# Performance work log

Hardware: AMD Instinct MI355X
Metric: run time of the kernel (lower is better)

Reference implementation:

```python
import jax, jax.numpy as jnp
import numpy as np

# LIF hyperparameters (from the torch module's `parameters` dict)
C = 1.0            # C_Osc
THR = 1.0          # v_Osc_threshold
BS = 256           # trials_per_stimulus
N = 512            # neurons_n
N_IN = 512         # n_in
TAU_SYN = 0.01     # tau_Osc_Ie
TAU_SYN_REC = 0.01 # tau_Osc_Irec
TAU_NEU = 0.02     # tau_Osc
GAIN_SYN = 1.0     # TDE_to_Osc_current
GAIN_SYN_REC = 0.5 # gain_syn_rec
DT = 0.001         # clock_sim
VR = 0.0           # reset_osc
I_MIN = 0.0        # I_minimum_osc
I_STEP = 0.01      # I_step_osc
REFRAC = 0.002     # refrac_Osc
REFR = REFRAC / DT # refractory period in steps
T = 500            # simulated timesteps


def spike(x):
    # SurrGradSpike.forward: hard threshold (surrogate grad only matters in bwd)
    return (x > 0.0).astype(x.dtype)


def setup_inputs() -> dict:
    key = jax.random.key(0)
    k1, k2, k3 = jax.random.split(key, 3)
    x = jax.random.uniform(k1, (T, BS, N_IN), dtype=jnp.float32)
    # train=True init: h1 ~ N(1, (std*0.5/sqrt(n_in))^2), r1 ~ N(0, same)
    std = 1.0 * 0.5 / np.sqrt(N_IN)
    h1 = 1.0 + std * jax.random.normal(k2, (N_IN, N), dtype=jnp.float32)
    r1 = std * jax.random.normal(k3, (N, N), dtype=jnp.float32)
    return {"x": x, "h1": h1, "r1": r1}


def reference(x, h1, r1):
    steady = I_MIN + I_STEP * jnp.arange(N, dtype=jnp.float32)  # [N]

    def step(state, x_t):
        V, Isyn, Irec, cnt, spk = state
        Isyn = Isyn - DT * Isyn / TAU_SYN + GAIN_SYN * (x_t @ h1)
        Irec = Irec - DT * Irec / TAU_SYN_REC + GAIN_SYN_REC * (spk @ r1)
        V = V + DT * (-V / TAU_NEU + (Isyn + Irec + steady) / C)
        V = jnp.maximum(V, 0.0)
        spk_new = spike(V - THR)
        cnt = REFR * spk_new + (1.0 - spk_new) * (cnt - 1.0)
        V = (1.0 - spk_new) * V * (cnt <= 0.0).astype(V.dtype) + spk_new * VR
        return (V, Isyn, Irec, cnt, spk_new), spk_new

    init = (
        jnp.ones((BS, N), jnp.float32),   # V
        jnp.zeros((BS, N), jnp.float32),  # Isyn
        jnp.zeros((BS, N), jnp.float32),  # Irec
        jnp.zeros((BS, N), jnp.float32),  # count_refr
        jnp.zeros((BS, N), jnp.float32),  # spk
    )
    _, spikes = jax.lax.scan(step, init, x)
    return spikes  # [T, BS, N]
```

## Files before the change

### kernel.cpp

```cpp
#include <hip/hip_runtime.h>

typedef __attribute__((ext_vector_type(8))) short short8;
typedef __attribute__((ext_vector_type(4))) float f32x4;

constexpr int BSZ = 256;
constexpr int NRN = 512;
constexpr int KIN = 512;
constexpr int TT  = 500;
constexpr int KT  = 32;
constexpr int BM2 = 64;
constexpr int NB2 = TT * BSZ / BM2;
constexpr int BM  = 128;
constexpr int BN  = 128;
constexpr int NBLK = (TT * BSZ / BM) * (NRN / BN);
constexpr size_t WS_NEED = (size_t)2 * KIN * NRN * sizeof(unsigned short);
constexpr unsigned long long FULLM = 0xFFFFFFFFFFFFFFFFULL;

__device__ __forceinline__ unsigned short bf16rne(float f) {
    unsigned u = __float_as_uint(f);
    u += 0x7FFFu + ((u >> 16) & 1u);
    return (unsigned short)(u >> 16);
}
__device__ __forceinline__ float bf16f(unsigned short s) {
    return __uint_as_float(((unsigned)s) << 16);
}
__device__ __forceinline__ unsigned cvtpk(float a, float b) {
    unsigned r;
    asm("v_cvt_pk_bf16_f32 %0, %1, %2" : "=v"(r) : "v"(a), "v"(b));
    return r;
}

__global__ __launch_bounds__(512)
void split_h(const float* __restrict__ h1,
             unsigned short* __restrict__ wsH,
             unsigned short* __restrict__ wsL)
{
    const int k = blockIdx.x;
    const int n = threadIdx.x;
    const float v = h1[(size_t)k * NRN + n];
    const unsigned short h  = bf16rne(v);
    const unsigned short lo = bf16rne(v - bf16f(h));
    const size_t byte = ((size_t)(k >> 3) * 512 + n) * 16 + (k & 7) * 2;
    *reinterpret_cast<unsigned short*>((char*)wsH + byte) = h;
    *reinterpret_cast<unsigned short*>((char*)wsL + byte) = lo;
}

__global__ __launch_bounds__(512, 4)
void lif_gemm2(const float* __restrict__ x,
               const unsigned short* __restrict__ wsH,
               const unsigned short* __restrict__ wsL,
               float* __restrict__ out)
{
    __shared__ short AhS[BM2 * KT], AlS[BM2 * KT];

    const int tid  = threadIdx.x;
    const int l    = tid & 63;
    const int w    = tid >> 6;
    const int wm   = (w >> 2) * 32;
    const int wn   = (w & 3) * 128;
    const int lrow = l & 15;
    const int loct = l >> 4;

    const int nid = (blockIdx.x & 7) * (NB2 / 8) + (blockIdx.x >> 3);
    const size_t m0 = (size_t)nid * BM2;

    const int arow  = tid >> 3;
    const int aslot = tid & 7;
    const int abyte = (arow * 64 + aslot * 8) ^ (((arow >> 1) & 3) << 4);

    f32x4 acc[2][8];
    #pragma unroll
    for (int i = 0; i < 2; ++i)
        #pragma unroll
        for (int j = 0; j < 8; ++j) acc[i][j] = (f32x4)0.0f;

    for (int kt = 0; kt < KIN / KT; ++kt) {
        {
            const float4 xv = *reinterpret_cast<const float4*>(
                x + (m0 + arow) * KIN + kt * KT + aslot * 4);
            const unsigned h01 = cvtpk(xv.x, xv.y);
            const unsigned h23 = cvtpk(xv.z, xv.w);
            const float r0  = xv.x - __uint_as_float(h01 << 16);
            const float r1v = xv.y - __uint_as_float(h01 & 0xFFFF0000u);
            const float r2  = xv.z - __uint_as_float(h23 << 16);
            const float r3  = xv.w - __uint_as_float(h23 & 0xFFFF0000u);
            const unsigned l01 = cvtpk(r0, r1v);
            const unsigned l23 = cvtpk(r2, r3);
            const unsigned long long hb = (unsigned long long)h01 | ((unsigned long long)h23 << 32);
            const unsigned long long lb = (unsigned long long)l01 | ((unsigned long long)l23 << 32);
            *reinterpret_cast<unsigned long long*>((char*)AhS + abyte) = hb;
            *reinterpret_cast<unsigned long long*>((char*)AlS + abyte) = lb;
        }
        __syncthreads();

        short8 ah[2], al[2];
        #pragma unroll
        for (int mi = 0; mi < 2; ++mi) {
            const int row  = wm + mi * 16 + lrow;
            const int byte = (row * 64 + loct * 16) ^ (((row >> 1) & 3) << 4);
            ah[mi] = *reinterpret_cast<const short8*>((const char*)AhS + byte);
            al[mi] = *reinterpret_cast<const short8*>((const char*)AlS + byte);
        }

        __builtin_amdgcn_s_setprio(1);
        #pragma unroll
        for (int ni = 0; ni < 8; ++ni) {
            const size_t bb = ((size_t)(kt * 4 + loct) * 512 + wn + ni * 16 + lrow) * 16;
            const short8 bh = *reinterpret_cast<const short8*>((const char*)wsH + bb);
            const short8 bl = *reinterpret_cast<const short8*>((const char*)wsL + bb);
            #pragma unroll
            for (int mi = 0; mi < 2; ++mi) {
                acc[mi][ni] = __builtin_amdgcn_mfma_f32_16x16x32_bf16(ah[mi], bh, acc[mi][ni], 0, 0, 0);
                acc[mi][ni] = __builtin_amdgcn_mfma_f32_16x16x32_bf16(ah[mi], bl, acc[mi][ni], 0, 0, 0);
                acc[mi][ni] = __builtin_amdgcn_mfma_f32_16x16x32_bf16(al[mi], bh, acc[mi][ni], 0, 0, 0);
            }
        }
        __builtin_amdgcn_s_setprio(0);
        __syncthreads();
    }

    #pragma unroll
    for (int mi = 0; mi < 2; ++mi)
        #pragma unroll
        for (int j = 0; j < 4; ++j) {
            const size_t row = m0 + wm + mi * 16 + loct * 4 + j;
            float* op = out + row * NRN + wn + lrow;
            #pragma unroll
            for (int ni = 0; ni < 8; ++ni)
                op[ni * 16] = acc[mi][ni][j];
        }
}

__global__ __launch_bounds__(256)
void lif_gemm_fb(const float* __restrict__ x,
                 const float* __restrict__ h1,
                 float* __restrict__ out)
{
    __shared__ short AhS[BM * KT], AlS[BM * KT], BhS[BN * KT], BlS[BN * KT];

    const int tid  = threadIdx.x;
    const int l    = tid & 63;
    const int w    = tid >> 6;
    const int wm   = (w & 1) * 64;
    const int wn   = (w >> 1) * 64;
    const int lrow = l & 15;
    const int loct = l >> 4;

    const int nid = (blockIdx.x & 7) * (NBLK / 8) + (blockIdx.x >> 3);
    const size_t m0 = (size_t)(nid >> 2) * BM;
    const int    n0 = (nid & 3) * BN;

    f32x4 acc[4][4];
    #pragma unroll
    for (int i = 0; i < 4; ++i)
        #pragma unroll
        for (int j = 0; j < 4; ++j) acc[i][j] = (f32x4)0.0f;

    for (int kt = 0; kt < KIN / KT; ++kt) {
        #pragma unroll
        for (int u2 = 0; u2 < 2; ++u2) {
            const int u = u2 * 256 + tid;
            const int nl = u & 127, koct = u >> 7;
            short8 hh, hl;
            #pragma unroll
            for (int i = 0; i < 8; ++i) {
                const float v = h1[(size_t)(kt * KT + koct * 8 + i) * NRN + n0 + nl];
                const unsigned short h = bf16rne(v);
                hh[i] = (short)h;
                hl[i] = (short)bf16rne(v - bf16f(h));
            }
            const int byte = (nl * 64 + koct * 16) ^ (((nl >> 1) & 3) << 4);
            *reinterpret_cast<short8*>((char*)BhS + byte) = hh;
            *reinterpret_cast<short8*>((char*)BlS + byte) = hl;
        }
        #pragma unroll
        for (int u4 = 0; u4 < 4; ++u4) {
            const int u = u4 * 256 + tid;
            const int row = u >> 3, slot = u & 7;
            const float4 xv = *reinterpret_cast<const float4*>(
                x + (m0 + row) * KIN + kt * KT + slot * 4);
            const unsigned h01 = cvtpk(xv.x, xv.y);
            const unsigned h23 = cvtpk(xv.z, xv.w);
            const float r0  = xv.x - __uint_as_float(h01 << 16);
            const float r1v = xv.y - __uint_as_float(h01 & 0xFFFF0000u);
            const float r2  = xv.z - __uint_as_float(h23 << 16);
            const float r3  = xv.w - __uint_as_float(h23 & 0xFFFF0000u);
            const unsigned l01 = cvtpk(r0, r1v);
            const unsigned l23 = cvtpk(r2, r3);
            const unsigned long long hb = (unsigned long long)h01 | ((unsigned long long)h23 << 32);
            const unsigned long long lb = (unsigned long long)l01 | ((unsigned long long)l23 << 32);
            const int byte = (row * 64 + slot * 8) ^ (((row >> 1) & 3) << 4);
            *reinterpret_cast<unsigned long long*>((char*)AhS + byte) = hb;
            *reinterpret_cast<unsigned long long*>((char*)AlS + byte) = lb;
        }
        __syncthreads();

        short8 ah[4], al[4], bh[4], bl[4];
        #pragma unroll
        for (int mi = 0; mi < 4; ++mi) {
            const int row  = wm + mi * 16 + lrow;
            const int byte = (row * 64 + loct * 16) ^ (((row >> 1) & 3) << 4);
            ah[mi] = *reinterpret_cast<const short8*>((const char*)AhS + byte);
            al[mi] = *reinterpret_cast<const short8*>((const char*)AlS + byte);
        }
        #pragma unroll
        for (int ni = 0; ni < 4; ++ni) {
            const int nn   = wn + ni * 16 + lrow;
            const int byte = (nn * 64 + loct * 16) ^ (((nn >> 1) & 3) << 4);
            bh[ni] = *reinterpret_cast<const short8*>((const char*)BhS + byte);
            bl[ni] = *reinterpret_cast<const short8*>((const char*)BlS + byte);
        }

        __builtin_amdgcn_s_setprio(1);
        #pragma unroll
        for (int mi = 0; mi < 4; ++mi)
            #pragma unroll
            for (int ni = 0; ni < 4; ++ni) {
                acc[mi][ni] = __builtin_amdgcn_mfma_f32_16x16x32_bf16(ah[mi], bh[ni], acc[mi][ni], 0, 0, 0);
                acc[mi][ni] = __builtin_amdgcn_mfma_f32_16x16x32_bf16(ah[mi], bl[ni], acc[mi][ni], 0, 0, 0);
                acc[mi][ni] = __builtin_amdgcn_mfma_f32_16x16x32_bf16(al[mi], bh[ni], acc[mi][ni], 0, 0, 0);
            }
        __builtin_amdgcn_s_setprio(0);
        __syncthreads();
    }

    #pragma unroll
    for (int mi = 0; mi < 4; ++mi)
        #pragma unroll
        for (int j = 0; j < 4; ++j) {
            const size_t row = m0 + wm + mi * 16 + loct * 4 + j;
            float* op = out + row * NRN + n0 + wn + lrow;
            #pragma unroll
            for (int ni = 0; ni < 4; ++ni)
                op[ni * 16] = acc[mi][ni][j];
        }
}

__global__ __launch_bounds__(512, 2)
void lif_scan(const float* __restrict__ r1,
              float* __restrict__ out)
{
    __shared__ unsigned long long smask[2][8];
    __shared__ unsigned long long flg[2];
    __shared__ unsigned long long vflg;

    const int n  = threadIdx.x;
    const int b  = blockIdx.x;
    const int wv = n >> 6;
    const int ln = n & 63;
    const size_t row = (size_t)b * NRN + n;
    constexpr size_t STEP = (size_t)BSZ * NRN;

    if (n < 16) ((unsigned long long*)smask)[n] = 0ULL;
    if (n < 2)  flg[n] = 0ULL;

    double csum = 0.0;
    for (int j = 0; j < KIN; ++j)
        csum += (double)r1[(size_t)j * NRN + n];

    double V = 1.0, Is = 0.0, Ir = 0.0, cnt = 0.0;
    const double steady = 0.01 * (double)n;
    constexpr double kS = 0.1, kN = 0.05, DT = 0.001;

    float cur[8], nxt[8];
    #pragma unroll
    for (int i = 0; i < 8; ++i) cur[i] = out[(size_t)i * STEP + row];
    __syncthreads();

#define STD_STEP(T, AREG)                                                     \
    {                                                                         \
        const int t_ = (T);                                                   \
        const int p_ = t_ & 1;                                                \
        const unsigned long long f_ = flg[p_];                                \
        double aR;                                                            \
        if (f_ == FULLM) {                                                    \
            aR = csum;                                                        \
        } else if (f_ == 0ULL) {                                              \
            aR = 0.0;                                                         \
        } else {                                                              \
            aR = 0.0;                                                         \
            _Pragma("unroll")                                                 \
            for (int w = 0; w < 8; ++w) {                                     \
                unsigned long long m_ = smask[p_][w];                         \
                while (m_) {                                 \
                    const int j = w * 64 + __builtin_ctzll(m_);               \
                    aR += (double)r1[(size_t)j * NRN + n];                    \
                    m_ &= m_ - 1;                                             \
                }                                                             \
            }                                                                 \
        }                                                                     \
        Is = Is - kS * Is + (double)(AREG);                 \
        Ir = Ir - kS * Ir + 0.5 * aR;                       \
        double Vn = V - kN * V + DT * (Is + Ir + steady);                     \
        Vn = fmax(Vn, 0.0);                                                   \
        const bool sp = (Vn - 1.0) > 0.0;                                     \
        cnt = sp ? 2.0 : (cnt - 1.0);                           \
        V = sp ? 0.0 : ((cnt <= 0.0) ? Vn : 0.0);                             \
        out[(size_t)t_ * STEP + row] = sp ? 1.0f : 0.0f;                      \
        const unsigned long long bal = __ballot(sp);                          \
        if (ln == 0) {                                                        \
            smask[p_ ^ 1][wv] = bal;                                          \
            const unsigned char fb =                                          \
                (bal == FULLM) ? 0xFFu : ((bal == 0ULL) ? 0x00u : 0x01u);     \
            ((unsigned char*)&flg[p_ ^ 1])[wv] = fb;                          \
        }                                                                     \
        __syncthreads();                                                      \
    }

    for (int t0 = 0; t0 < 496; t0 += 8) {
        #pragma unroll
        for (int i = 0; i < 8; ++i)
            nxt[i] = (t0 + 8 + i < TT) ? out[(size_t)(t0 + 8 + i) * STEP + row] : 0.0f;

        if (flg[t0 & 1] == FULLM) {
            const double Vc = V, Isc = Is, Irc = Ir, cc = cnt;
            bool allm = true;
            #pragma unroll
            for (int i = 0; i < 8; ++i) {
                Is = Is - kS * Is + (double)cur[i];
                Ir = Ir - kS * Ir + 0.5 * csum;
                double Vn = V - kN * V + DT * (Is + Ir + steady);
                Vn = fmax(Vn, 0.0);
                const bool sp = (Vn - 1.0) > 0.0;
                allm &= sp;
                cnt = sp ? 2.0 : (cnt - 1.0);
                V = sp ? 0.0 : ((cnt <= 0.0) ? Vn : 0.0);
                out[(size_t)(t0 + i) * STEP + row] = sp ? 1.0f : 0.0f;
            }
            const unsigned long long bal = __ballot(allm);
            if (ln == 0) {
                ((unsigned char*)&vflg)[wv] = (bal == FULLM) ? 0xFFu : 0x00u;
                smask[t0 & 1][wv] = FULLM;
                ((unsigned char*)&flg[t0 & 1])[wv] = 0xFFu;
            }
            __syncthreads();
            if (vflg != FULLM) {
                V = Vc; Is = Isc; Ir = Irc; cnt = cc;
                STD_STEP(t0 + 0, cur[0])
                STD_STEP(t0 + 1, cur[1])
                STD_STEP(t0 + 2, cur[2])
                STD_STEP(t0 + 3, cur[3])
                STD_STEP(t0 + 4, cur[4])
                STD_STEP(t0 + 5, cur[5])
                STD_STEP(t0 + 6, cur[6])
                STD_STEP(t0 + 7, cur[7])
            }
        } else {
            STD_STEP(t0 + 0, cur[0])
            STD_STEP(t0 + 1, cur[1])
            STD_STEP(t0 + 2, cur[2])
            STD_STEP(t0 + 3, cur[3])
            STD_STEP(t0 + 4, cur[4])
            STD_STEP(t0 + 5, cur[5])
            STD_STEP(t0 + 6, cur[6])
            STD_STEP(t0 + 7, cur[7])
        }

        #pragma unroll
        for (int i = 0; i < 8; ++i) cur[i] = nxt[i];
    }

    STD_STEP(496, cur[0])
    STD_STEP(497, cur[1])
    STD_STEP(498, cur[2])
    STD_STEP(499, cur[3])
#undef STD_STEP
}

extern "C" void kernel_launch(void* const* d_in, const int* in_sizes, int n_in,
                              void* d_out, int out_size, void* d_ws, size_t ws_size,
                              hipStream_t stream) {
    const float* x  = (const float*)d_in[0];
    const float* h1 = (const float*)d_in[1];
    const float* r1 = (const float*)d_in[2];
    float* out = (float*)d_out;
    (void)in_sizes; (void)n_in; (void)out_size;

    if (ws_size >= WS_NEED) {
        unsigned short* wsH = (unsigned short*)d_ws;
        unsigned short* wsL = wsH + (size_t)KIN * NRN;
        split_h<<<dim3(KIN), dim3(NRN), 0, stream>>>(h1, wsH, wsL);
        lif_gemm2<<<dim3(NB2), dim3(512), 0, stream>>>(x, wsH, wsL, out);
    } else {
        lif_gemm_fb<<<dim3(NBLK), dim3(256), 0, stream>>>(x, h1, out);
    }
    lif_scan<<<dim3(BSZ), dim3(512), 0, stream>>>(r1, out);
}
```

Baseline: 393.2 us.

## Restructure input GEMM into double-buffered 128x128 tiles with staged, pre-swizzled weights

Replaces the 64-row, 512-wide GEMM kernel, which read bf16 weight fragments straight from global memory on every k-step, with 128x128 tiles. Each k-step's weight slab is staged into LDS from a workspace the split kernel now writes in the LDS swizzle order, so it can be copied directly. A two-stage LDS ping-pong prefetches the next x and weight slabs into registers while the MFMAs on the current slab run, removing one barrier per step. In exchange, x is re-read by four column blocks instead of once, and more LDS and registers are used per block, which can lower occupancy.

```diff
diff --git a/kernel.cpp b/kernel.cpp
--- a/kernel.cpp
+++ b/kernel.cpp
@@ -7,11 +7,9 @@
 constexpr int NRN = 512;
 constexpr int KIN = 512;
 constexpr int TT  = 500;
-constexpr int KT  = 32;
-constexpr int BM2 = 64;
-constexpr int NB2 = TT * BSZ / BM2;
 constexpr int BM  = 128;
 constexpr int BN  = 128;
+constexpr int KT  = 32;
 constexpr int NBLK = (TT * BSZ / BM) * (NRN / BN);
 constexpr size_t WS_NEED = (size_t)2 * KIN * NRN * sizeof(unsigned short);
 constexpr unsigned long long FULLM = 0xFFFFFFFFFFFFFFFFULL;
@@ -40,44 +38,58 @@
     const float v = h1[(size_t)k * NRN + n];
     const unsigned short h  = bf16rne(v);
     const unsigned short lo = bf16rne(v - bf16f(h));
-    const size_t byte = ((size_t)(k >> 3) * 512 + n) * 16 + (k & 7) * 2;
+    const int kt = k >> 5, koct = (k >> 3) & 3, i = k & 7;
+    const int nb = n >> 7, nl = n & 127;
+    const int byte = (kt * 4 + nb) * 8192 +
+                     ((nl * 64 + koct * 16) ^ (((nl >> 1) & 3) << 4)) + i * 2;
     *reinterpret_cast<unsigned short*>((char*)wsH + byte) = h;
     *reinterpret_cast<unsigned short*>((char*)wsL + byte) = lo;
 }
 
-__global__ __launch_bounds__(512, 4)
-void lif_gemm2(const float* __restrict__ x,
-               const unsigned short* __restrict__ wsH,
-               const unsigned short* __restrict__ wsL,
-               float* __restrict__ out)
+__global__ __launch_bounds__(256)
+void lif_gemm_ps(const float* __restrict__ x,
+                 const unsigned short* __restrict__ wsH,
+                 const unsigned short* __restrict__ wsL,
+                 float* __restrict__ out)
 {
-    __shared__ short AhS[BM2 * KT], AlS[BM2 * KT];
+    __shared__ short AhS[2][BM * KT], AlS[2][BM * KT];
+    __shared__ short BhS[2][BN * KT], BlS[2][BN * KT];
 
     const int tid  = threadIdx.x;
     const int l    = tid & 63;
     const int w    = tid >> 6;
-    const int wm   = (w >> 2) * 32;
-    const int wn   = (w & 3) * 128;
+    const int wm   = (w & 1) * 64;
+    const int wn   = (w >> 1) * 64;
     const int lrow = l & 15;
     const int loct = l >> 4;
 
-    const int nid = (blockIdx.x & 7) * (NB2 / 8) + (blockIdx.x >> 3);
-    const size_t m0 = (size_t)nid * BM2;
-
-    const int arow  = tid >> 3;
-    const int aslot = tid & 7;
-    const int abyte = (arow * 64 + aslot * 8) ^ (((arow >> 1) & 3) << 4);
-
-    f32x4 acc[2][8];
+    const int nid = (blockIdx.x & 7) * (NBLK / 8) + (blockIdx.x >> 3);
+    const size_t m0 = (size_t)(nid >> 2) * BM;
+    const int    nb = nid & 3;
+
+    f32x4 acc[4][4];
     #pragma unroll
-    for (int i = 0; i < 2; ++i)
-        #pragma unroll
-        for (int j = 0; j < 8; ++j) acc[i][j] = (f32x4)0.0f;
-
-    for (int kt = 0; kt < KIN / KT; ++kt) {
-        {
+    for (int i = 0; i < 4; ++i)
+        #pragma unroll
+        for (int j = 0; j < 4; ++j) acc[i][j] = (f32x4)0.0f;
+
+    {
+        const char* sH = (const char*)wsH + nb * 8192;
+        const char* sL = (const char*)wsL + nb * 8192;
+        *reinterpret_cast<float4*>((char*)BhS[0] + tid * 16) =
+            *reinterpret_cast<const float4*>(sH + tid * 16);
+        *reinterpret_cast<float4*>((char*)BhS[0] + 4096 + tid * 16) =
+            *reinterpret_cast<const float4*>(sH + 4096 + tid * 16);
+        *reinterpret_cast<float4*>((char*)BlS[0] + tid * 16) =
+            *reinterpret_cast<const float4*>(sL + tid * 16);
+        *reinterpret_cast<float4*>((char*)BlS[0] + 4096 + tid * 16) =
+            *reinterpret_cast<const float4*>(sL + 4096 + tid * 16);
+        #pragma unroll
+        for (int u4 = 0; u4 < 4; ++u4) {
+            const int u = u4 * 256 + tid;
+            const int row = u >> 3, slot = u & 7;
             const float4 xv = *reinterpret_cast<const float4*>(
-                x + (m0 + arow) * KIN + kt * KT + aslot * 4);
+                x + (m0 + row) * KIN + slot * 4);
             const unsigned h01 = cvtpk(xv.x, xv.y);
             const unsigned h23 = cvtpk(xv.z, xv.w);
             const float r0  = xv.x - __uint_as_float(h01 << 16);
@@ -88,45 +100,102 @@
             const unsigned l23 = cvtpk(r2, r3);
             const unsigned long long hb = (unsigned long long)h01 | ((unsigned long long)h23 << 32);
             const unsigned long long lb = (unsigned long long)l01 | ((unsigned long long)l23 << 32);
-            *reinterpret_cast<unsigned long long*>((char*)AhS + abyte) = hb;
-            *reinterpret_cast<unsigned long long*>((char*)AlS + abyte) = lb;
-        }
-        __syncthreads();
-
-        short8 ah[2], al[2];
-        #pragma unroll
-        for (int mi = 0; mi < 2; ++mi) {
+            const int byte = (row * 64 + slot * 8) ^ (((row >> 1) & 3) << 4);
+            *reinterpret_cast<unsigned long long*>((char*)AhS[0] + byte) = hb;
+            *reinterpret_cast<unsigned long long*>((char*)AlS[0] + byte) = lb;
+        }
+    }
+    __syncthreads();
+
+    for (int kt = 0; kt < KIN / KT; ++kt) {
+        const int p = kt & 1;
+
+        float4 xr0, xr1, xr2, xr3, bh0, bh1, bl0, bl1;
+        const bool more = (kt + 1 < KIN / KT);
+        if (more) {
+            const int ktn = kt + 1;
+            const char* sH = (const char*)wsH + (ktn * 4 + nb) * 8192;
+            const char* sL = (const char*)wsL + (ktn * 4 + nb) * 8192;
+            bh0 = *reinterpret_cast<const float4*>(sH + tid * 16);
+            bh1 = *reinterpret_cast<const float4*>(sH + 4096 + tid * 16);
+            bl0 = *reinterpret_cast<const float4*>(sL + tid * 16);
+            bl1 = *reinterpret_cast<const float4*>(sL + 4096 + tid * 16);
+            const int u0 = tid, u1 = 256 + tid, u2 = 512 + tid, u3 = 768 + tid;
+            xr0 = *reinterpret_cast<const float4*>(
+                x + (m0 + (u0 >> 3)) * KIN + ktn * KT + (u0 & 7) * 4);
+            xr1 = *reinterpret_cast<const float4*>(
+                x + (m0 + (u1 >> 3)) * KIN + ktn * KT + (u1 & 7) * 4);
+            xr2 = *reinterpret_cast<const float4*>(
+                x + (m0 + (u2 >> 3)) * KIN + ktn * KT + (u2 & 7) * 4);
+            xr3 = *reinterpret_cast<const float4*>(
+                x + (m0 + (u3 >> 3)) * KIN + ktn * KT + (u3 & 7) * 4);
+        }
+
+        short8 ah[4], al[4], bh[4], bl[4];
+        #pragma unroll
+        for (int mi = 0; mi < 4; ++mi) {
             const int row  = wm + mi * 16 + lrow;
             const int byte = (row * 64 + loct * 16) ^ (((row >> 1) & 3) << 4);
-            ah[mi] = *reinterpret_cast<const short8*>((const char*)AhS + byte);
-            al[mi] = *reinterpret_cast<const short8*>((const char*)AlS + byte);
+            ah[mi] = *reinterpret_cast<const short8*>((const char*)AhS[p] + byte);
+            al[mi] = *reinterpret_cast<const short8*>((const char*)AlS[p] + byte);
+        }
+        #pragma unroll
+        for (int ni = 0; ni < 4; ++ni) {
+            const int nn   = wn + ni * 16 + lrow;
+            const int byte = (nn * 64 + loct * 16) ^ (((nn >> 1) & 3) << 4);
+            bh[ni] = *reinterpret_cast<const short8*>((const char*)BhS[p] + byte);
+            bl[ni] = *reinterpret_cast<const short8*>((const char*)BlS[p] + byte);
         }
 
         __builtin_amdgcn_s_setprio(1);
         #pragma unroll
-        for (int ni = 0; ni < 8; ++ni) {
-            const size_t bb = ((size_t)(kt * 4 + loct) * 512 + wn + ni * 16 + lrow) * 16;
-            const short8 bh = *reinterpret_cast<const short8*>((const char*)wsH + bb);
-            const short8 bl = *reinterpret_cast<const short8*>((const char*)wsL + bb);
-            #pragma unroll
-            for (int mi = 0; mi < 2; ++mi) {
-                acc[mi][ni] = __builtin_amdgcn_mfma_f32_16x16x32_bf16(ah[mi], bh, acc[mi][ni], 0, 0, 0);
-                acc[mi][ni] = __builtin_amdgcn_mfma_f32_16x16x32_bf16(ah[mi], bl, acc[mi][ni], 0, 0, 0);
-                acc[mi][ni] = __builtin_amdgcn_mfma_f32_16x16x32_bf16(al[mi], bh, acc[mi][ni], 0, 0, 0);
-            }
-        }
+        for (int mi = 0; mi < 4; ++mi)
+            #pragma unroll
+            for (int ni = 0; ni < 4; ++ni) {
+                acc[mi][ni] = __builtin_amdgcn_mfma_f32_16x16x32_bf16(ah[mi], bh[ni], acc[mi][ni], 0, 0, 0);
+                acc[mi][ni] = __builtin_amdgcn_mfma_f32_16x16x32_bf16(ah[mi], bl[ni], acc[mi][ni], 0, 0, 0);
+                acc[mi][ni] = __builtin_amdgcn_mfma_f32_16x16x32_bf16(al[mi], bh[ni], acc[mi][ni], 0, 0, 0);
+            }
         __builtin_amdgcn_s_setprio(0);
+
+        if (more) {
+            const int q = p ^ 1;
+            *reinterpret_cast<float4*>((char*)BhS[q] + tid * 16)        = bh0;
+            *reinterpret_cast<float4*>((char*)BhS[q] + 4096 + tid * 16) = bh1;
+            *reinterpret_cast<float4*>((char*)BlS[q] + tid * 16)        = bl0;
+            *reinterpret_cast<float4*>((char*)BlS[q] + 4096 + tid * 16) = bl1;
+            const float4 xrs[4] = { xr0, xr1, xr2, xr3 };
+            #pragma unroll
+            for (int u4 = 0; u4 < 4; ++u4) {
+                const int u = u4 * 256 + tid;
+                const int row = u >> 3, slot = u & 7;
+                const float4 xv = xrs[u4];
+                const unsigned h01 = cvtpk(xv.x, xv.y);
+                const unsigned h23 = cvtpk(xv.z, xv.w);
+                const float r0  = xv.x - __uint_as_float(h01 << 16);
+                const float r1v = xv.y - __uint_as_float(h01 & 0xFFFF0000u);
+                const float r2  = xv.z - __uint_as_float(h23 << 16);
+                const float r3  = xv.w - __uint_as_float(h23 & 0xFFFF0000u);
+                const unsigned l01 = cvtpk(r0, r1v);
+                const unsigned l23 = cvtpk(r2, r3);
+                const unsigned long long hb = (unsigned long long)h01 | ((unsigned long long)h23 << 32);
+                const unsigned long long lb = (unsigned long long)l01 | ((unsigned long long)l23 << 32);
+                const int byte = (row * 64 + slot * 8) ^ (((row >> 1) & 3) << 4);
+                *reinterpret_cast<unsigned long long*>((char*)AhS[q] + byte) = hb;
+                *reinterpret_cast<unsigned long long*>((char*)AlS[q] + byte) = lb;
+            }
+        }
         __syncthreads();
     }
 
     #pragma unroll
-    for (int mi = 0; mi < 2; ++mi)
+    for (int mi = 0; mi < 4; ++mi)
         #pragma unroll
         for (int j = 0; j < 4; ++j) {
             const size_t row = m0 + wm + mi * 16 + loct * 4 + j;
-            float* op = out + row * NRN + wn + lrow;
-            #pragma unroll
-            for (int ni = 0; ni < 8; ++ni)
+            float* op = out + row * NRN + nb * BN + wn + lrow;
+            #pragma unroll
+            for (int ni = 0; ni < 4; ++ni)
                 op[ni * 16] = acc[mi][ni][j];
         }
 }
@@ -380,7 +449,7 @@
         unsigned short* wsH = (unsigned short*)d_ws;
         unsigned short* wsL = wsH + (size_t)KIN * NRN;
         split_h<<<dim3(KIN), dim3(NRN), 0, stream>>>(h1, wsH, wsL);
-        lif_gemm2<<<dim3(NB2), dim3(512), 0, stream>>>(x, wsH, wsL, out);
+        lif_gemm_ps<<<dim3(NBLK), dim3(256), 0, stream>>>(x, wsH, wsL, out);
     } else {
         lif_gemm_fb<<<dim3(NBLK), dim3(256), 0, stream>>>(x, h1, out);
     }
```

New measurement: 347.1 us. -11.7%, faster.
